# Kernel optimization log

Measured on AMD Instinct MI355X. Metric: run time of the kernel, lower is better.

## Reference

```python
import jax, jax.numpy as jnp
import numpy as np


def setup_inputs() -> dict:
    key = jax.random.key(0)
    k1, k2, k3, k4, k5 = jax.random.split(key, 5)
    B, C, V, D, O = 8, 64, 25000, 12, 64
    x = jax.random.normal(k1, (B, C, V), dtype=jnp.float32)
    nbr_idx = jax.random.randint(k2, (B, V, D), 0, V, dtype=jnp.int32)
    # true 1-ring valence in [1, D]
    deg = jax.random.randint(k3, (B, V), 1, D + 1, dtype=jnp.int32)
    # conv weight [O, C, 1, 2] flattened to [O, C, 2], fan-in init scale
    W = jax.random.normal(k4, (O, C, 2), dtype=jnp.float32) * (1.0 / np.sqrt(C * 2))
    b = jax.random.normal(k5, (O,), dtype=jnp.float32) * 0.01
    return {"x": x, "nbr_idx": nbr_idx, "deg": deg, "W": W, "b": b}


def reference(x, nbr_idx, deg, W, b):
    # x: [B, C, V]; nbr_idx: [B, V, D] padded 1-ring; deg: [B, V] valid count
    B, C, V = x.shape
    D = nbr_idx.shape[-1]
    # gather neighbor features: [B, C, V, D]
    gathered = jax.vmap(lambda xb, ib: xb[:, ib])(x, nbr_idx)
    mask = (jnp.arange(D, dtype=deg.dtype)[None, None, :] < deg[:, :, None])  # [B, V, D]
    maskf = mask.astype(x.dtype)[:, None, :, :]  # [B, 1, V, D]
    denom = jnp.maximum(deg, 1).astype(x.dtype)[:, None, :]  # [B, 1, V]
    nbr_mean = jnp.sum(gathered * maskf, axis=-1) / denom  # [B, C, V]
    # G: [B, C, V, 2] = (self feature, 1-ring mean); conv2d kernel (1,2)
    G = jnp.stack([x, nbr_mean], axis=-1)
    out = jnp.einsum('bcvk,ock->bov', G, W) + b[None, :, None]
    return out[..., None]  # [B, O, V, 1]
```

## Files before the change

kernel.cpp:

```cpp
#include <hip/hip_runtime.h>
#include <stdint.h>


#define NB 8
#define NC 64
#define NV 25000
#define ND 12
#define NO 64
#define GT 391
#define GVT 782

typedef uint32_t u32x4 __attribute__((ext_vector_type(4)));
typedef uint32_t u32x2 __attribute__((ext_vector_type(2)));
typedef __bf16  bf16x8 __attribute__((ext_vector_type(8)));
typedef float   f32x4  __attribute__((ext_vector_type(4)));

__device__ inline uint32_t bf16pack(float a, float b) {
    uint32_t ua = __float_as_uint(a), ub = __float_as_uint(b);
    ua = (ua + 0x7fffu + ((ua >> 16) & 1u)) >> 16;
    ub = (ub + 0x7fffu + ((ub >> 16) & 1u)) >> 16;
    return ua | (ub << 16);
}
__device__ inline float blo(uint32_t u) { return __uint_as_float(u << 16); }
__device__ inline float bhi(uint32_t u) { return __uint_as_float(u & 0xffff0000u); }

__global__ __launch_bounds__(256) void wt_kernel(const float* __restrict__ W,
                                                 uint32_t* __restrict__ Wcb) {
    int i = blockIdx.x * 256 + threadIdx.x;
    int m = i >> 5;
    int c = (i & 31) * 2;
    int k = m >> 6;
    int o = m & 63;
    float s0 = W[o * (NC * 2) + c * 2 + k];
    float s1 = W[o * (NC * 2) + (c + 1) * 2 + k];
    Wcb[i] = bf16pack(s0, s1);
}

__global__ __launch_bounds__(256) void ygemm_mfma(const float* __restrict__ x,
                                                  const uint32_t* __restrict__ Wcb,
                                                  const float* __restrict__ bias,
                                                  uint32_t* __restrict__ y0,
                                                  uint32_t* __restrict__ y1) {
    const int b = blockIdx.x & 7;
    const int tile = blockIdx.x >> 3;
    const int wave = threadIdx.x >> 6;
    const int lane = threadIdx.x & 63;
    const int l15 = lane & 15;
    const int lq = lane >> 4;
    const int v = tile * 64 + wave * 16 + l15;
    const int vc = v < NV ? v : NV - 1;
    const float* xb = x + (size_t)b * NC * NV;

    union BU { uint32_t u[4]; bf16x8 v; } bu[2];
#pragma unroll
    for (int kt = 0; kt < 2; ++kt) {
        const float* xc = xb + (size_t)(kt * 32 + lq * 8) * NV + vc;
#pragma unroll
        for (int jp = 0; jp < 4; ++jp) {
            float s0 = __builtin_nontemporal_load(xc + (size_t)(2 * jp) * NV);
            float s1 = __builtin_nontemporal_load(xc + (size_t)(2 * jp + 1) * NV);
            bu[kt].u[jp] = bf16pack(s0, s1);
        }
    }

    f32x4 acc[8];
#pragma unroll
    for (int mt = 0; mt < 8; ++mt) acc[mt] = (f32x4){0.f, 0.f, 0.f, 0.f};

#pragma unroll
    for (int mt = 0; mt < 8; ++mt) {
#pragma unroll
        for (int kt = 0; kt < 2; ++kt) {
            union { u32x4 q; bf16x8 v; } au;
            au.q = *(const u32x4*)(Wcb + (size_t)(mt * 16 + l15) * 32 + kt * 16 + lq * 4);
            acc[mt] = __builtin_amdgcn_mfma_f32_16x16x32_bf16(au.v, bu[kt].v, acc[mt], 0, 0, 0);
        }
    }

    if (v < NV) {
        uint32_t* yr0 = y0 + ((size_t)b * NV + v) * 32;
        uint32_t* yr1 = y1 + ((size_t)b * NV + v) * 32;
#pragma unroll
        for (int mt = 0; mt < 8; ++mt) {
            const int mo = mt * 16 + lq * 4;
            f32x4 a = acc[mt];
            if (mt < 4) {
                const float* bp = bias + mo;
                a[0] += bp[0]; a[1] += bp[1]; a[2] += bp[2]; a[3] += bp[3];
                u32x2 p = {bf16pack(a[0], a[1]), bf16pack(a[2], a[3])};
                __builtin_nontemporal_store(p, (u32x2*)(yr0 + (mo >> 1)));
            } else {
                u32x2 p = {bf16pack(a[0], a[1]), bf16pack(a[2], a[3])};
                *(u32x2*)(yr1 + ((mo - 64) >> 1)) = p;
            }
        }
    }
}

__global__ __launch_bounds__(256) void gather_out(const int* __restrict__ nbr,
                                                  const int* __restrict__ deg,
                                                  const uint32_t* __restrict__ y0,
                                                  const uint32_t* __restrict__ y1,
                                                  float* __restrict__ out) {
    __shared__ float lds[32 * 68];

    const int b = blockIdx.x & 7;
    const int tile = blockIdx.x >> 3;
    const int lane = threadIdx.x & 63;
    const int wave = threadIdx.x >> 6;
    const int s = lane >> 3;
    const int j = lane & 7;
    const int vloc = wave * 8 + s;
    const int v = tile * 32 + vloc;
    const int vc = v < NV ? v : NV - 1;
    const size_t bv = (size_t)b * NV + vc;

    int idxr[ND];
    {
        const int4* p = reinterpret_cast<const int4*>(nbr + bv * ND);
        int4 a0 = p[0], a1 = p[1], a2 = p[2];
        idxr[0] = a0.x; idxr[1] = a0.y; idxr[2]  = a0.z; idxr[3]  = a0.w;
        idxr[4] = a1.x; idxr[5] = a1.y; idxr[6]  = a1.z; idxr[7]  = a1.w;
        idxr[8] = a2.x; idxr[9] = a2.y; idxr[10] = a2.z; idxr[11] = a2.w;
    }
    const int dg = deg[bv];
    const float inv = 1.0f / (float)dg;
    const uint32_t* y1b = y1 + (size_t)b * NV * 32;

    u32x4 su = __builtin_nontemporal_load(
        reinterpret_cast<const u32x4*>(y0 + bv * 32) + j);

    u32x4 rows[ND];
#pragma unroll
    for (int d = 0; d < ND; ++d) {
        if (d < dg)
            rows[d] = *(reinterpret_cast<const u32x4*>(y1b + (size_t)idxr[d] * 32) + j);
    }

    float ns[8];
#pragma unroll
    for (int t = 0; t < 8; ++t) ns[t] = 0.0f;
#pragma unroll
    for (int d = 0; d < ND; ++d) {
        if (d < dg) {
            u32x4 u = rows[d];
            ns[0] += blo(u[0]); ns[1] += bhi(u[0]);
            ns[2] += blo(u[1]); ns[3] += bhi(u[1]);
            ns[4] += blo(u[2]); ns[5] += bhi(u[2]);
            ns[6] += blo(u[3]); ns[7] += bhi(u[3]);
        }
    }

    {
        float f[8];
        f[0] = __builtin_fmaf(inv, ns[0], blo(su[0]));
        f[1] = __builtin_fmaf(inv, ns[1], bhi(su[0]));
        f[2] = __builtin_fmaf(inv, ns[2], blo(su[1]));
        f[3] = __builtin_fmaf(inv, ns[3], bhi(su[1]));
        f[4] = __builtin_fmaf(inv, ns[4], blo(su[2]));
        f[5] = __builtin_fmaf(inv, ns[5], bhi(su[2]));
        f[6] = __builtin_fmaf(inv, ns[6], blo(su[3]));
        f[7] = __builtin_fmaf(inv, ns[7], bhi(su[3]));
        f32x4 w0 = {f[0], f[1], f[2], f[3]};
        f32x4 w1 = {f[4], f[5], f[6], f[7]};
        *reinterpret_cast<f32x4*>(&lds[vloc * 68 + j * 8])     = w0;
        *reinterpret_cast<f32x4*>(&lds[vloc * 68 + j * 8 + 4]) = w1;
    }
    __syncthreads();

    {
        const int vl = threadIdx.x & 31;
        const int o8 = threadIdx.x >> 5;
        const int vv = tile * 32 + vl;
        if (vv < NV) {
            float* ob = out + (size_t)b * NO * NV + vv;
#pragma unroll
            for (int oo = 0; oo < 8; ++oo) {
                const int o = oo * 8 + o8;
                __builtin_nontemporal_store(lds[vl * 68 + o], ob + (size_t)o * NV);
            }
        }
    }
}

__global__ __launch_bounds__(64) void fallback_kernel(const float* __restrict__ x,
                                                      const int* __restrict__ nbr,
                                                      const int* __restrict__ deg,
                                                      const float* __restrict__ W,
                                                      const float* __restrict__ bias,
                                                      float* __restrict__ out) {
    const int bvi = blockIdx.x;
    const int b = bvi / NV, v = bvi % NV;
    const int o = threadIdx.x;
    const int degv = deg[bvi];
    const float inv = 1.0f / (float)degv;
    float acc = bias[o];
    for (int c = 0; c < NC; ++c) {
        const float* xc = x + ((size_t)b * NC + c) * NV;
        float m = 0.0f;
        for (int d = 0; d < degv; ++d) m += xc[nbr[(size_t)bvi * ND + d]];
        acc += W[o * (NC * 2) + c * 2] * xc[v] + W[o * (NC * 2) + c * 2 + 1] * (m * inv);
    }
    out[((size_t)b * NO + o) * NV + v] = acc;
}

extern "C" void kernel_launch(void* const* d_in, const int* in_sizes, int n_in,
                              void* d_out, int out_size, void* d_ws, size_t ws_size,
                              hipStream_t stream) {
    const float* x    = (const float*)d_in[0];
    const int*   nbr  = (const int*)d_in[1];
    const int*   deg  = (const int*)d_in[2];
    const float* W    = (const float*)d_in[3];
    const float* bias = (const float*)d_in[4];
    float* out = (float*)d_out;

    const size_t wcb_dw = 4096;
    const size_t yplane = (size_t)NB * NV * 32;
    const size_t need = (wcb_dw + 2 * yplane) * 4;
    if (ws_size >= need) {
        uint32_t* Wcb = (uint32_t*)d_ws;
        uint32_t* y0 = Wcb + wcb_dw;
        uint32_t* y1 = y0 + yplane;
        wt_kernel<<<dim3(16), 256, 0, stream>>>(W, Wcb);
        ygemm_mfma<<<dim3(NB * GT), 256, 0, stream>>>(x, Wcb, bias, y0, y1);
        gather_out<<<dim3(NB * GVT), 256, 0, stream>>>(nbr, deg, y0, y1, out);
    } else {
        fallback_kernel<<<dim3(NB * NV), 64, 0, stream>>>(x, nbr, deg, W, bias, out);
    }
}
```

Measured before the change: 177.2 us.

## Stage x tile through LDS and reuse W fragments across two vertex subtiles

The GEMM kernel now loads a 128-vertex tile of x with fully coalesced per-channel reads, packs it to bf16 into shared memory, then reads the MFMA B fragments from LDS. Each wave handles two 16-vertex subtiles, so every W fragment load feeds two MFMAs, and the grid is halved. The aim is better global-load coalescing and less W reload traffic, at the cost of an LDS round trip, a barrier and more accumulator registers.

```diff
diff --git a/kernel.cpp b/kernel.cpp
--- a/kernel.cpp
+++ b/kernel.cpp
@@ -7,7 +7,8 @@
 #define NV 25000
 #define ND 12
 #define NO 64
-#define GT 391
+#define VTILE 128
+#define NGT 196
 #define GVT 782
 
 typedef uint32_t u32x4 __attribute__((ext_vector_type(4)));
@@ -41,57 +42,80 @@
                                                   const float* __restrict__ bias,
                                                   uint32_t* __restrict__ y0,
                                                   uint32_t* __restrict__ y1) {
+    __shared__ uint32_t xt[VTILE * 36];
+
     const int b = blockIdx.x & 7;
     const int tile = blockIdx.x >> 3;
-    const int wave = threadIdx.x >> 6;
-    const int lane = threadIdx.x & 63;
-    const int l15 = lane & 15;
-    const int lq = lane >> 4;
-    const int v = tile * 64 + wave * 16 + l15;
-    const int vc = v < NV ? v : NV - 1;
+    const int vbase = tile * VTILE;
+    const int tid = threadIdx.x;
     const float* xb = x + (size_t)b * NC * NV;
 
-    union BU { uint32_t u[4]; bf16x8 v; } bu[2];
+    {
+        const int vl = tid & 127;
+        const int ph = tid >> 7;
+        int vg = vbase + vl;
+        if (vg >= NV) vg = NV - 1;
+#pragma unroll
+        for (int r = 0; r < 16; ++r) {
+            const int p = r * 2 + ph;
+            const int c = p * 2;
+            float s0 = __builtin_nontemporal_load(xb + (size_t)c * NV + vg);
+            float s1 = __builtin_nontemporal_load(xb + (size_t)(c + 1) * NV + vg);
+            xt[vl * 36 + p] = bf16pack(s0, s1);
+        }
+    }
+    __syncthreads();
+
+    const int lane = tid & 63, wave = tid >> 6;
+    const int l15 = lane & 15, lq = lane >> 4;
+
+    union BF { u32x4 q; bf16x8 v; } bf[2][2];
+#pragma unroll
+    for (int s = 0; s < 2; ++s) {
+        const int vloc = (wave * 2 + s) * 16 + l15;
+#pragma unroll
+        for (int kt = 0; kt < 2; ++kt)
+            bf[s][kt].q = *reinterpret_cast<const u32x4*>(&xt[vloc * 36 + kt * 16 + lq * 4]);
+    }
+
+    f32x4 acc[2][8];
+#pragma unroll
+    for (int s = 0; s < 2; ++s)
+#pragma unroll
+        for (int mt = 0; mt < 8; ++mt) acc[s][mt] = (f32x4){0.f, 0.f, 0.f, 0.f};
+
 #pragma unroll
     for (int kt = 0; kt < 2; ++kt) {
-        const float* xc = xb + (size_t)(kt * 32 + lq * 8) * NV + vc;
-#pragma unroll
-        for (int jp = 0; jp < 4; ++jp) {
-            float s0 = __builtin_nontemporal_load(xc + (size_t)(2 * jp) * NV);
-            float s1 = __builtin_nontemporal_load(xc + (size_t)(2 * jp + 1) * NV);
-            bu[kt].u[jp] = bf16pack(s0, s1);
-        }
-    }
-
-    f32x4 acc[8];
-#pragma unroll
-    for (int mt = 0; mt < 8; ++mt) acc[mt] = (f32x4){0.f, 0.f, 0.f, 0.f};
-
-#pragma unroll
-    for (int mt = 0; mt < 8; ++mt) {
-#pragma unroll
-        for (int kt = 0; kt < 2; ++kt) {
+#pragma unroll
+        for (int mt = 0; mt < 8; ++mt) {
             union { u32x4 q; bf16x8 v; } au;
             au.q = *(const u32x4*)(Wcb + (size_t)(mt * 16 + l15) * 32 + kt * 16 + lq * 4);
-            acc[mt] = __builtin_amdgcn_mfma_f32_16x16x32_bf16(au.v, bu[kt].v, acc[mt], 0, 0, 0);
-        }
-    }
-
-    if (v < NV) {
-        uint32_t* yr0 = y0 + ((size_t)b * NV + v) * 32;
-        uint32_t* yr1 = y1 + ((size_t)b * NV + v) * 32;
-#pragma unroll
-        for (int mt = 0; mt < 8; ++mt) {
-            const int mo = mt * 16 + lq * 4;
-            f32x4 a = acc[mt];
-            if (mt < 4) {
-                const float* bp = bias + mo;
-                a[0] += bp[0]; a[1] += bp[1]; a[2] += bp[2]; a[3] += bp[3];
-                u32x2 p = {bf16pack(a[0], a[1]), bf16pack(a[2], a[3])};
-                __builtin_nontemporal_store(p, (u32x2*)(yr0 + (mo >> 1)));
-            } else {
-                u32x2 p = {bf16pack(a[0], a[1]), bf16pack(a[2], a[3])};
-                *(u32x2*)(yr1 + ((mo - 64) >> 1)) = p;
+#pragma unroll
+            for (int s = 0; s < 2; ++s)
+                acc[s][mt] = __builtin_amdgcn_mfma_f32_16x16x32_bf16(au.v, bf[s][kt].v,
+                                                                     acc[s][mt], 0, 0, 0);
+        }
+    }
+
+#pragma unroll
+    for (int s = 0; s < 2; ++s) {
+        const int v = vbase + (wave * 2 + s) * 16 + l15;
+        if (v < NV) {
+            uint32_t* yr0 = y0 + ((size_t)b * NV + v) * 32;
+            uint32_t* yr1 = y1 + ((size_t)b * NV + v) * 32;
+#pragma unroll
+            for (int mt = 0; mt < 8; ++mt) {
+                const int mo = mt * 16 + lq * 4;
+                f32x4 a = acc[s][mt];
+                if (mt < 4) {
+                    const float* bp = bias + mo;
+                    a[0] += bp[0]; a[1] += bp[1]; a[2] += bp[2]; a[3] += bp[3];
+                    u32x2 p = {bf16pack(a[0], a[1]), bf16pack(a[2], a[3])};
+                    __builtin_nontemporal_store(p, (u32x2*)(yr0 + (mo >> 1)));
+                } else {
+                    u32x2 p = {bf16pack(a[0], a[1]), bf16pack(a[2], a[3])};
+                    *(u32x2*)(yr1 + ((mo - 64) >> 1)) = p;
+                }
             }
         }
     }
@@ -222,7 +246,7 @@
         uint32_t* y0 = Wcb + wcb_dw;
         uint32_t* y1 = y0 + yplane;
         wt_kernel<<<dim3(16), 256, 0, stream>>>(W, Wcb);
-        ygemm_mfma<<<dim3(NB * GT), 256, 0, stream>>>(x, Wcb, bias, y0, y1);
+        ygemm_mfma<<<dim3(NB * NGT), 256, 0, stream>>>(x, Wcb, bias, y0, y1);
         gather_out<<<dim3(NB * GVT), 256, 0, stream>>>(nbr, deg, y0, y1, out);
     } else {
         fallback_kernel<<<dim3(NB * NV), 64, 0, stream>>>(x, nbr, deg, W, bias, out);
```

After: 164.9 us. -6.9%, faster.
